# Optimization experiments

Hardware: AMD Instinct MI355X
Metric: run time of the kernel (lower is better)

The kernel has to match this reference:

```python
import jax, jax.numpy as jnp
import numpy as np

L = 12      # gpt2-small layers
D = 768     # n_embd
H = 12      # heads
NTOK = 60   # A5 group size / vocab
DST = 128   # d_state
B, T = 8, 1024
ID_ID = 0
INJECT = 8  # inject_layer


def _ln(x, g, b):
    m = x.mean(-1, keepdims=True)
    v = x.var(-1, keepdims=True)
    return (x - m) * jax.lax.rsqrt(v + 1e-5) * g + b


def _forward(tok_emb, state_emb, sp_w, sp_b, wh_w, wh_b, ws_w, ws_b, wd_w, wd_b,
             head_w, head_b, wpe, ln1_g, ln1_b, attn_w, attn_b, proj_w, proj_b,
             ln2_g, ln2_b, fc_w, fc_b, mproj_w, mproj_b, lnf_g, lnf_b,
             input_ids, mul):
    Bc, Tc = input_ids.shape
    # --- sequential group-recurrence state scan: s_{t+1} = mul[x_t, s_t] ---
    def step(s, ids_t):
        s2 = mul[ids_t, s]
        return s2, s2
    s0 = jnp.full((Bc,), ID_ID, jnp.int32)
    _, post = jax.lax.scan(step, s0, input_ids.T)   # [T, B] post-states
    post = post.T                                    # [B, T]
    pre = jnp.concatenate([jnp.full((Bc, 1), ID_ID, jnp.int32), post[:, :-1]], axis=1)
    # clean mode: inject PRE-states everywhere (mask == 1)
    s = state_emb[pre] @ sp_w + sp_b                 # [B, T, D] projected state channel
    # input_add injection
    x = tok_emb[input_ids] + s
    # --- frozen GPT-2 forward ---
    h = x + wpe[:Tc]
    hd = D // H
    scale = 1.0 / np.sqrt(hd)
    causal = jnp.tril(jnp.ones((Tc, Tc), bool))
    for l in range(L):
        a = _ln(h, ln1_g[l], ln1_b[l])
        qkv = a @ attn_w[l] + attn_b[l]
        q, k, v = jnp.split(qkv, 3, axis=-1)
        q = q.reshape(Bc, Tc, H, hd)
        k = k.reshape(Bc, Tc, H, hd)
        v = v.reshape(Bc, Tc, H, hd)
        sc = jnp.einsum('bthd,bshd->bhts', q, k) * scale
        sc = jnp.where(causal, sc, jnp.float32(-1e9))
        att = jax.nn.softmax(sc, axis=-1)
        o = jnp.einsum('bhts,bshd->bthd', att, v).reshape(Bc, Tc, D)
        h = h + o @ proj_w[l] + proj_b[l]
        m = _ln(h, ln2_g[l], ln2_b[l])
        h = h + jax.nn.gelu(m @ fc_w[l] + fc_b[l], approximate=True) @ mproj_w[l] + mproj_b[l]
        if l == INJECT:
            # gated residual fusion hook on block output
            gate = jax.nn.sigmoid(h @ wh_w + wh_b + s @ ws_w + ws_b)
            h = h + gate * (s @ wd_w + wd_b)
    h = _ln(h, lnf_g, lnf_b)
    logits = h[:, -1] @ head_w + head_b             # [B, NTOK]
    return logits


def setup_inputs() -> dict:
    key = jax.random.key(0)
    ks = iter(jax.random.split(key, 48))
    p = lambda *sh: (0.02 * jax.random.normal(next(ks), sh)).astype(jnp.float32)
    return dict(
        input_ids=jax.random.randint(next(ks), (B, T), 0, NTOK, jnp.int32),
        mul=jax.random.randint(next(ks), (NTOK, NTOK), 0, NTOK, jnp.int32),
        tok_emb=p(NTOK, D), state_emb=p(NTOK, DST),
        sp_w=p(DST, D), sp_b=jnp.zeros((D,), jnp.float32),
        wh_w=p(D, D), wh_b=jnp.zeros((D,), jnp.float32),
        ws_w=p(D, D), ws_b=jnp.zeros((D,), jnp.float32),
        wd_w=p(D, D), wd_b=jnp.zeros((D,), jnp.float32),
        head_w=p(D, NTOK), head_b=jnp.zeros((NTOK,), jnp.float32),
        wpe=p(T, D),
        ln1_g=jnp.ones((L, D), jnp.float32), ln1_b=jnp.zeros((L, D), jnp.float32),
        attn_w=p(L, D, 3 * D), attn_b=jnp.zeros((L, 3 * D), jnp.float32),
        proj_w=p(L, D, D), proj_b=jnp.zeros((L, D), jnp.float32),
        ln2_g=jnp.ones((L, D), jnp.float32), ln2_b=jnp.zeros((L, D), jnp.float32),
        fc_w=p(L, D, 4 * D), fc_b=jnp.zeros((L, 4 * D), jnp.float32),
        mproj_w=p(L, 4 * D, D), mproj_b=jnp.zeros((L, D), jnp.float32),
        lnf_g=jnp.ones((D,), jnp.float32), lnf_b=jnp.zeros((D,), jnp.float32),
    )


def reference(input_ids, mul, tok_emb, state_emb, sp_w, sp_b, wh_w, wh_b, ws_w, ws_b,
              wd_w, wd_b, head_w, head_b, wpe, ln1_g, ln1_b, attn_w, attn_b,
              proj_w, proj_b, ln2_g, ln2_b, fc_w, fc_b, mproj_w, mproj_b, lnf_g, lnf_b):
    return _forward(tok_emb, state_emb, sp_w, sp_b, wh_w, wh_b, ws_w, ws_b, wd_w, wd_b,
                    head_w, head_b, wpe, ln1_g, ln1_b, attn_w, attn_b, proj_w, proj_b,
                    ln2_g, ln2_b, fc_w, fc_b, mproj_w, mproj_b, lnf_g, lnf_b,
                    input_ids, mul)
```

## Files before the change

### kernel.cpp

```cpp
#include <hip/hip_runtime.h>
#include <hip/hip_bf16.h>
#include <math.h>

#define L_LAYERS 12
#define D_MODEL 768
#define H_HEADS 12
#define HD 64
#define NTOK 60
#define DST 128
#define BATCH 8
#define SEQ 1024
#define NT (BATCH * SEQ)
#define INJECT_L 8

typedef short bf16x8 __attribute__((ext_vector_type(8)));
typedef float f32x4 __attribute__((ext_vector_type(4)));
typedef unsigned short u16x4 __attribute__((ext_vector_type(4)));

__device__ __forceinline__ unsigned short f2bf(float f) {
    unsigned int u = __float_as_uint(f);
    u = (u + 0x7FFF + ((u >> 16) & 1)) >> 16;
    return (unsigned short)u;
}

__device__ __forceinline__ float gelu_fast(float x) {
    float two_c = 1.5957691216057308f * (x + 0.044715f * x * x * x);
    return x / (1.0f + __expf(-two_c));
}

__device__ __forceinline__ void async_copy16(void* lds, const void* gmem) {
    __builtin_amdgcn_global_load_lds(
        (const __attribute__((address_space(1))) unsigned int*)gmem,
        (__attribute__((address_space(3))) unsigned int*)lds,
        16, 0, 0);
}

__global__ __launch_bounds__(1024) void scan_kernel(const int* __restrict__ ids,
                                                    const int* __restrict__ mul,
                                                    int* __restrict__ pre) {
    __shared__ int smul[NTOK * NTOK];
    __shared__ int sids[SEQ];
    __shared__ int Mc[64 * NTOK];
    __shared__ int entry[64];
    int b = blockIdx.x;
    int tid = threadIdx.x;
    for (int i = tid; i < NTOK * NTOK; i += 1024) smul[i] = mul[i];
    for (int i = tid; i < SEQ; i += 1024) sids[i] = ids[b * SEQ + i];
    __syncthreads();
    for (int task = tid; task < 64 * NTOK; task += 1024) {
        int c = task / NTOK, s = task - c * NTOK;
        int st = s;
        #pragma unroll
        for (int j = 0; j < 16; j++) st = smul[sids[c * 16 + j] * NTOK + st];
        Mc[c * NTOK + s] = st;
    }
    __syncthreads();
    if (tid == 0) {
        int st = 0;
        for (int c = 0; c < 64; c++) { entry[c] = st; st = Mc[c * NTOK + st]; }
    }
    __syncthreads();
    if (tid < 64) {
        int c = tid;
        int st = entry[c];
        int* pr = pre + b * SEQ + c * 16;
        #pragma unroll
        for (int j = 0; j < 16; j++) {
            pr[j] = st;
            st = smul[sids[c * 16 + j] * NTOK + st];
        }
    }
}

__global__ __launch_bounds__(256) void state_table_kernel(const float* __restrict__ state_emb,
                                                          const float* __restrict__ sp_w,
                                                          const float* __restrict__ sp_b,
                                                          float* __restrict__ stable) {
    int st = blockIdx.x;
    __shared__ float se[DST];
    if (threadIdx.x < DST) se[threadIdx.x] = state_emb[st * DST + threadIdx.x];
    __syncthreads();
    for (int d = threadIdx.x; d < D_MODEL; d += 256) {
        float acc = sp_b[d];
        #pragma unroll 8
        for (int k = 0; k < DST; k++) acc += se[k] * sp_w[k * D_MODEL + d];
        stable[st * D_MODEL + d] = acc;
    }
}

__global__ __launch_bounds__(64) void embed_gather(const int* __restrict__ ids,
                                                   const int* __restrict__ pre,
                                                   const float* __restrict__ tok_emb,
                                                   const float* __restrict__ stable,
                                                   const float* __restrict__ wpe,
                                                   unsigned short* __restrict__ s_bf,
                                                   float* __restrict__ h) {
    int n = blockIdx.x;
    int t = n & (SEQ - 1);
    int lane = threadIdx.x;
    const float4* te = (const float4*)(tok_emb + (size_t)ids[n] * D_MODEL);
    const float4* sv = (const float4*)(stable + (size_t)pre[n] * D_MODEL);
    const float4* wp = (const float4*)(wpe + (size_t)t * D_MODEL);
    float4* hr = (float4*)(h + (size_t)n * D_MODEL);
    unsigned short* sr = s_bf + (size_t)n * D_MODEL;
    #pragma unroll
    for (int j = 0; j < 3; j++) {
        int idx = j * 64 + lane;
        float4 a = te[idx], b = sv[idx], c = wp[idx];
        float4 o;
        o.x = a.x + b.x + c.x; o.y = a.y + b.y + c.y;
        o.z = a.z + b.z + c.z; o.w = a.w + b.w + c.w;
        hr[idx] = o;
        u16x4 pk = { f2bf(b.x), f2bf(b.y), f2bf(b.z), f2bf(b.w) };
        *(u16x4*)&sr[idx * 4] = pk;
    }
}

__global__ __launch_bounds__(256) void ln_bf16_kernel(const float* __restrict__ x,
                                                      const float* __restrict__ g,
                                                      const float* __restrict__ bta,
                                                      unsigned short* __restrict__ out) {
    int row = blockIdx.x * 4 + (threadIdx.x >> 6);
    int lane = threadIdx.x & 63;
    const float4* xr = (const float4*)(x + (size_t)row * D_MODEL);
    float4 v[3];
    float sum = 0.f, sq = 0.f;
    #pragma unroll
    for (int j = 0; j < 3; j++) {
        v[j] = xr[j * 64 + lane];
        sum += v[j].x + v[j].y + v[j].z + v[j].w;
        sq += v[j].x * v[j].x + v[j].y * v[j].y + v[j].z * v[j].z + v[j].w * v[j].w;
    }
    for (int off = 32; off; off >>= 1) {
        sum += __shfl_xor(sum, off);
        sq += __shfl_xor(sq, off);
    }
    float mean = sum * (1.0f / D_MODEL);
    float var = sq * (1.0f / D_MODEL) - mean * mean;
    float r = rsqrtf(var + 1e-5f);
    const float4* g4 = (const float4*)g;
    const float4* b4 = (const float4*)bta;
    unsigned short* orow = out + (size_t)row * D_MODEL;
    #pragma unroll
    for (int j = 0; j < 3; j++) {
        int idx = j * 64 + lane;
        float4 gg = g4[idx], bb = b4[idx];
        u16x4 pk = { f2bf((v[j].x - mean) * r * gg.x + bb.x),
                     f2bf((v[j].y - mean) * r * gg.y + bb.y),
                     f2bf((v[j].z - mean) * r * gg.z + bb.z),
                     f2bf((v[j].w - mean) * r * gg.w + bb.w) };
        *(u16x4*)&orow[idx * 4] = pk;
    }
}

__global__ __launch_bounds__(256) void ln_f32_kernel(const float* __restrict__ x,
                                                     const float* __restrict__ g,
                                                     const float* __restrict__ bta,
                                                     float* __restrict__ out,
                                                     long in_stride, long out_stride) {
    long row = blockIdx.x;
    const float* xr = x + row * in_stride;
    int tid = threadIdx.x;
    float v0 = xr[tid], v1 = xr[tid + 256], v2 = xr[tid + 512];
    float sum = v0 + v1 + v2;
    float sq = v0 * v0 + v1 * v1 + v2 * v2;
    for (int off = 32; off; off >>= 1) {
        sum += __shfl_xor(sum, off);
        sq += __shfl_xor(sq, off);
    }
    __shared__ float red[8];
    int wid = tid >> 6;
    if ((tid & 63) == 0) { red[wid] = sum; red[4 + wid] = sq; }
    __syncthreads();
    sum = red[0] + red[1] + red[2] + red[3];
    sq = red[4] + red[5] + red[6] + red[7];
    float mean = sum * (1.0f / D_MODEL);
    float var = sq * (1.0f / D_MODEL) - mean * mean;
    float r = rsqrtf(var + 1e-5f);
    float* orow = out + row * out_stride;
    orow[tid] = (v0 - mean) * r * g[tid] + bta[tid];
    orow[tid + 256] = (v1 - mean) * r * g[tid + 256] + bta[tid + 256];
    orow[tid + 512] = (v2 - mean) * r * g[tid + 512] + bta[tid + 512];
}

__device__ __forceinline__ void conv_tile(const float* __restrict__ src,
                                          unsigned short* __restrict__ dst,
                                          int R, int C, int rt, int ct,
                                          int tc, int tr) {
    __shared__ float tile[32][33];
    int r0 = rt * 32, c0 = ct * 32;
    #pragma unroll
    for (int i = 0; i < 32; i += 8)
        tile[tr + i][tc] = src[(size_t)(r0 + tr + i) * C + c0 + tc];
    __syncthreads();
    #pragma unroll
    for (int i = 0; i < 32; i += 8)
        dst[(size_t)(c0 + tr + i) * R + r0 + tc] = f2bf(tile[tc][tr + i]);
}

__global__ __launch_bounds__(256) void wconv_layer(const float* __restrict__ attn_w,
                                                   const float* __restrict__ proj_w,
                                                   const float* __restrict__ fc_w,
                                                   const float* __restrict__ mproj_w,
                                                   unsigned short* __restrict__ attn_wt,
                                                   unsigned short* __restrict__ proj_wt,
                                                   unsigned short* __restrict__ fc_wt,
                                                   unsigned short* __restrict__ mproj_wt) {
    int bid = blockIdx.x;
    const float* src; unsigned short* dst; int R, C, CT, tloc;
    if (bid < 1728)      { src = attn_w;  dst = attn_wt;  R = 768;  C = 2304; CT = 72; tloc = bid; }
    else if (bid < 2304) { src = proj_w;  dst = proj_wt;  R = 768;  C = 768;  CT = 24; tloc = bid - 1728; }
    else if (bid < 4608) { src = fc_w;    dst = fc_wt;    R = 768;  C = 3072; CT = 96; tloc = bid - 2304; }
    else                 { src = mproj_w; dst = mproj_wt; R = 3072; C = 768;  CT = 24; tloc = bid - 4608; }
    int rt = tloc / CT, ct = tloc - rt * CT;
    conv_tile(src, dst, R, C, rt, ct, threadIdx.x, threadIdx.y);
}

__global__ __launch_bounds__(256) void wconv_inject(const float* __restrict__ wh_w,
                                                    const float* __restrict__ ws_w,
                                                    const float* __restrict__ wd_w,
                                                    unsigned short* __restrict__ wh_t,
                                                    unsigned short* __restrict__ ws_t,
                                                    unsigned short* __restrict__ wd_t) {
    int bid = blockIdx.x;
    int sel = bid / 576, tloc = bid - sel * 576;
    const float* src = sel == 0 ? wh_w : (sel == 1 ? ws_w : wd_w);
    unsigned short* dst = sel == 0 ? wh_t : (sel == 1 ? ws_t : wd_t);
    int rt = tloc / 24, ct = tloc - rt * 24;
    conv_tile(src, dst, 768, 768, rt, ct, threadIdx.x, threadIdx.y);
}

#define FLAG_OUTBF16 1
#define FLAG_GELU 2
#define FLAG_RESID 4
#define FLAG_MIRROR 8

__global__ __launch_bounds__(256) void mfma_gemm(const unsigned short* __restrict__ A,
                                                 const unsigned short* __restrict__ Wt,
                                                 const float* __restrict__ bias,
                                                 const float* __restrict__ residual,
                                                 float* __restrict__ Cf,
                                                 unsigned short* __restrict__ Cb,
                                                 unsigned short* __restrict__ Cmir,
                                                 int M, int K, int N, int flags) {
    __shared__ unsigned short As[128 * 64];
    __shared__ unsigned short Bs[128 * 64];
    int tid = threadIdx.x;
    int wave = tid >> 6, lane = tid & 63;
    int quad = lane >> 4, l16 = lane & 15;
    int m0 = blockIdx.x * 128, n0 = blockIdx.y * 128;
    int wm = (wave & 1) * 64, wn = (wave >> 1) * 64;
    f32x4 acc[4][4] = {};

    for (int k0 = 0; k0 < K; k0 += 64) {
        #pragma unroll
        for (int i = 0; i < 4; i++) {
            int chunk = i * 256 + wave * 64 + lane;
            int r = chunk >> 3;
            int cc = (chunk & 7) ^ (r & 7);
            async_copy16(&As[(i * 256 + wave * 64) * 8],
                         A + (size_t)(m0 + r) * K + k0 + cc * 8);
            async_copy16(&Bs[(i * 256 + wave * 64) * 8],
                         Wt + (size_t)(n0 + r) * K + k0 + cc * 8);
        }
        __syncthreads();
        #pragma unroll
        for (int sub = 0; sub < 2; sub++) {
            bf16x8 af[4], bfr[4];
            #pragma unroll
            for (int mi = 0; mi < 4; mi++) {
                int R = wm + mi * 16 + l16;
                int slot = (sub * 4 + quad) ^ (R & 7);
                af[mi] = *(const bf16x8*)&As[R * 64 + slot * 8];
            }
            #pragma unroll
            for (int ni = 0; ni < 4; ni++) {
                int R = wn + ni * 16 + l16;
                int slot = (sub * 4 + quad) ^ (R & 7);
                bfr[ni] = *(const bf16x8*)&Bs[R * 64 + slot * 8];
            }
            #pragma unroll
            for (int mi = 0; mi < 4; mi++)
                #pragma unroll
                for (int ni = 0; ni < 4; ni++)
                    acc[mi][ni] = __builtin_amdgcn_mfma_f32_16x16x32_bf16(
                        af[mi], bfr[ni], acc[mi][ni], 0, 0, 0);
        }
        __syncthreads();
    }
    #pragma unroll
    for (int mi = 0; mi < 4; mi++) {
        #pragma unroll
        for (int ni = 0; ni < 4; ni++) {
            int col = n0 + wn + ni * 16 + l16;
            float bv = bias[col];
            #pragma unroll
            for (int r = 0; r < 4; r++) {
                int row = m0 + wm + mi * 16 + quad * 4 + r;
                size_t idx = (size_t)row * N + col;
                float v = acc[mi][ni][r] + bv;
                if (flags & FLAG_RESID) v += residual[idx];
                if (flags & FLAG_GELU) v = gelu_fast(v);
                if (flags & FLAG_OUTBF16) Cb[idx] = f2bf(v);
                else Cf[idx] = v;
                if (flags & FLAG_MIRROR) Cmir[idx] = f2bf(v);
            }
        }
    }
}

__global__ __launch_bounds__(256) void attn_mfma(const unsigned short* __restrict__ qkv,
                                                 unsigned short* __restrict__ o) {
    int qt = gridDim.x - 1 - blockIdx.x;
    int hh = blockIdx.y, b = blockIdx.z;
    int tid = threadIdx.x, wave = tid >> 6, lane = tid & 63;
    int quad = lane >> 4, l16 = lane & 15;
    __shared__ unsigned short Qs[64][72];
    __shared__ unsigned short Ks[64][72];
    __shared__ unsigned short Vt[64][72];
    __shared__ unsigned short Ps[4][16][72];
    const size_t rstride = 3 * D_MODEL;
    int q0 = qt * 64;

    {
        size_t qbase = ((size_t)(b * SEQ + q0)) * rstride + hh * HD;
        #pragma unroll
        for (int i = 0; i < 2; i++) {
            int chunk = i * 256 + tid;
            int r = chunk >> 3, cc = chunk & 7;
            *(uint4*)&Qs[r][cc * 8] =
                *(const uint4*)(qkv + qbase + (size_t)r * rstride + cc * 8);
        }
    }

    float m_r[4] = {-1e30f, -1e30f, -1e30f, -1e30f};
    float l_r[4] = {0.f, 0.f, 0.f, 0.f};
    f32x4 oacc[4] = {};

    for (int kt = 0; kt <= qt; kt++) {
        int kb = kt * 64;
        __syncthreads();
        size_t kbase = ((size_t)(b * SEQ + kb)) * rstride + D_MODEL + hh * HD;
        size_t vbase = ((size_t)(b * SEQ + kb)) * rstride + 2 * D_MODEL + hh * HD;
        #pragma unroll
        for (int i = 0; i < 2; i++) {
            int chunk = i * 256 + tid;
            int r = chunk >> 3, cc = chunk & 7;
            *(uint4*)&Ks[r][cc * 8] =
                *(const uint4*)(qkv + kbase + (size_t)r * rstride + cc * 8);
        }
        #pragma unroll
        for (int i = 0; i < 2; i++) {
            int key = lane;
            int dg = i * 4 + wave;
            uint4 vv = *(const uint4*)(qkv + vbase + (size_t)key * rstride + dg * 8);
            const unsigned short* vs = (const unsigned short*)&vv;
            #pragma unroll
            for (int j = 0; j < 8; j++) Vt[dg * 8 + j][key] = vs[j];
        }
        __syncthreads();

        f32x4 sacc[4] = {};
        bf16x8 qf0 = *(const bf16x8*)&Qs[wave * 16 + l16][quad * 8];
        bf16x8 qf1 = *(const bf16x8*)&Qs[wave * 16 + l16][32 + quad * 8];
        #pragma unroll
        for (int ni = 0; ni < 4; ni++) {
            bf16x8 kf0 = *(const bf16x8*)&Ks[ni * 16 + l16][quad * 8];
            bf16x8 kf1 = *(const bf16x8*)&Ks[ni * 16 + l16][32 + quad * 8];
            sacc[ni] = __builtin_amdgcn_mfma_f32_16x16x32_bf16(qf0, kf0, sacc[ni], 0, 0, 0);
            sacc[ni] = __builtin_amdgcn_mfma_f32_16x16x32_bf16(qf1, kf1, sacc[ni], 0, 0, 0);
        }

        bool diag = (kt == qt);
        const float scale = 0.125f;
        #pragma unroll
        for (int r = 0; r < 4; r++) {
            int qrow_loc = wave * 16 + quad * 4 + r;
            float mx = m_r[r];
            #pragma unroll
            for (int ni = 0; ni < 4; ni++) {
                float sv = sacc[ni][r] * scale;
                if (diag && (ni * 16 + l16 > qrow_loc)) sv = -1e30f;
                sacc[ni][r] = sv;
                mx = fmaxf(mx, sv);
            }
            for (int off = 8; off; off >>= 1) mx = fmaxf(mx, __shfl_xor(mx, off));
            float alpha = __expf(m_r[r] - mx);
            m_r[r] = mx;
            float ls = 0.f;
            #pragma unroll
            for (int ni = 0; ni < 4; ni++) {
                float p = __expf(sacc[ni][r] - mx);
                sacc[ni][r] = p;
                ls += p;
            }
            for (int off = 8; off; off >>= 1) ls += __shfl_xor(ls, off);
            l_r[r] = l_r[r] * alpha + ls;
            #pragma unroll
            for (int ni = 0; ni < 4; ni++) oacc[ni][r] *= alpha;
        }

        #pragma unroll
        for (int ni = 0; ni < 4; ni++)
            #pragma unroll
            for (int r = 0; r < 4; r++)
                Ps[wave][quad * 4 + r][ni * 16 + l16] = f2bf(sacc[ni][r]);
        asm volatile("s_waitcnt lgkmcnt(0)" ::: "memory");

        bf16x8 pf0 = *(const bf16x8*)&Ps[wave][l16][quad * 8];
        bf16x8 pf1 = *(const bf16x8*)&Ps[wave][l16][32 + quad * 8];
        #pragma unroll
        for (int ni = 0; ni < 4; ni++) {
            bf16x8 vf0 = *(const bf16x8*)&Vt[ni * 16 + l16][quad * 8];
            bf16x8 vf1 = *(const bf16x8*)&Vt[ni * 16 + l16][32 + quad * 8];
            oacc[ni] = __builtin_amdgcn_mfma_f32_16x16x32_bf16(pf0, vf0, oacc[ni], 0, 0, 0);
            oacc[ni] = __builtin_amdgcn_mfma_f32_16x16x32_bf16(pf1, vf1, oacc[ni], 0, 0, 0);
        }
    }

    #pragma unroll
    for (int ni = 0; ni < 4; ni++) {
        #pragma unroll
        for (int r = 0; r < 4; r++) {
            float inv = 1.0f / l_r[r];
            int row = q0 + wave * 16 + quad * 4 + r;
            o[((size_t)(b * SEQ + row)) * D_MODEL + hh * HD + ni * 16 + l16] =
                f2bf(oacc[ni][r] * inv);
        }
    }
}

__global__ __launch_bounds__(256) void gate_kernel(float* __restrict__ h,
                                                   const float* __restrict__ z,
                                                   const float* __restrict__ dv,
                                                   size_t total) {
    size_t i = (size_t)blockIdx.x * blockDim.x + threadIdx.x;
    size_t stride = (size_t)gridDim.x * blockDim.x;
    for (; i < total; i += stride) {
        float g = 1.0f / (1.0f + __expf(-z[i]));
        h[i] += g * dv[i];
    }
}

__global__ __launch_bounds__(64) void head_kernel(const float* __restrict__ hn,
                                                  const float* __restrict__ head_w,
                                                  const float* __restrict__ head_b,
                                                  float* __restrict__ out) {
    int b = blockIdx.x;
    int n = threadIdx.x;
    if (n < NTOK) {
        float acc = head_b[n];
        const float* hr = hn + b * D_MODEL;
        for (int k = 0; k < D_MODEL; k++) acc += hr[k] * head_w[k * NTOK + n];
        out[b * NTOK + n] = acc;
    }
}

extern "C" void kernel_launch(void* const* d_in, const int* in_sizes, int n_in,
                              void* d_out, int out_size, void* d_ws, size_t ws_size,
                              hipStream_t stream) {
    (void)in_sizes; (void)n_in; (void)out_size; (void)ws_size;
    const int* input_ids = (const int*)d_in[0];
    const int* mul       = (const int*)d_in[1];
    const float* tok_emb = (const float*)d_in[2];
    const float* state_emb = (const float*)d_in[3];
    const float* sp_w = (const float*)d_in[4];
    const float* sp_b = (const float*)d_in[5];
    const float* wh_w = (const float*)d_in[6];
    const float* wh_b = (const float*)d_in[7];
    const float* ws_w = (const float*)d_in[8];
    const float* ws_b = (const float*)d_in[9];
    const float* wd_w = (const float*)d_in[10];
    const float* wd_b = (const float*)d_in[11];
    const float* head_w = (const float*)d_in[12];
    const float* head_b = (const float*)d_in[13];
    const float* wpe  = (const float*)d_in[14];
    const float* ln1_g = (const float*)d_in[15];
    const float* ln1_b = (const float*)d_in[16];
    const float* attn_w = (const float*)d_in[17];
    const float* attn_b = (const float*)d_in[18];
    const float* proj_w = (const float*)d_in[19];
    const float* proj_b = (const float*)d_in[20];
    const float* ln2_g = (const float*)d_in[21];
    const float* ln2_b = (const float*)d_in[22];
    const float* fc_w = (const float*)d_in[23];
    const float* fc_b = (const float*)d_in[24];
    const float* mproj_w = (const float*)d_in[25];
    const float* mproj_b = (const float*)d_in[26];
    const float* lnf_g = (const float*)d_in[27];
    const float* lnf_b = (const float*)d_in[28];
    float* out = (float*)d_out;

    size_t off = 0;
    auto alloc = [&](size_t bytes) {
        void* p = (char*)d_ws + off;
        off += (bytes + 255) & ~(size_t)255;
        return p;
    };
    int* pre = (int*)alloc((size_t)NT * 4);
    float* stable = (float*)alloc((size_t)NTOK * D_MODEL * 4);
    unsigned short* s_bf   = (unsigned short*)alloc((size_t)NT * D_MODEL * 2);
    float* h               = (float*)alloc((size_t)NT * D_MODEL * 4);
    unsigned short* a_bf   = (unsigned short*)alloc((size_t)NT * D_MODEL * 2);
    unsigned short* qkv_bf = (unsigned short*)alloc((size_t)NT * 3 * D_MODEL * 2);
    unsigned short* u_bf   = (unsigned short*)alloc((size_t)NT * 4 * D_MODEL * 2);
    unsigned short* h8_bf  = (unsigned short*)alloc((size_t)NT * D_MODEL * 2);
    float* z  = (float*)alloc((size_t)NT * D_MODEL * 4);
    float* dv = (float*)alloc((size_t)NT * D_MODEL * 4);
    float* hn = (float*)alloc((size_t)BATCH * D_MODEL * 4);
    unsigned short* attn_wt  = (unsigned short*)alloc((size_t)2304 * 768 * 2);
    unsigned short* proj_wt  = (unsigned short*)alloc((size_t)768 * 768 * 2);
    unsigned short* fc_wt    = (unsigned short*)alloc((size_t)3072 * 768 * 2);
    unsigned short* mproj_wt = (unsigned short*)alloc((size_t)768 * 3072 * 2);
    unsigned short* wh_t = (unsigned short*)alloc((size_t)768 * 768 * 2);
    unsigned short* ws_t = (unsigned short*)alloc((size_t)768 * 768 * 2);
    unsigned short* wd_t = (unsigned short*)alloc((size_t)768 * 768 * 2);

    scan_kernel<<<BATCH, 1024, 0, stream>>>(input_ids, mul, pre);
    state_table_kernel<<<NTOK, 256, 0, stream>>>(state_emb, sp_w, sp_b, stable);
    embed_gather<<<NT, 64, 0, stream>>>(input_ids, pre, tok_emb, stable, wpe, s_bf, h);
    wconv_inject<<<1728, dim3(32, 8), 0, stream>>>(wh_w, ws_w, wd_w, wh_t, ws_t, wd_t);

    for (int l = 0; l < L_LAYERS; l++) {
        wconv_layer<<<6912, dim3(32, 8), 0, stream>>>(
            attn_w + (size_t)l * 768 * 2304, proj_w + (size_t)l * 768 * 768,
            fc_w + (size_t)l * 768 * 3072, mproj_w + (size_t)l * 3072 * 768,
            attn_wt, proj_wt, fc_wt, mproj_wt);

        ln_bf16_kernel<<<NT / 4, 256, 0, stream>>>(h, ln1_g + l * D_MODEL,
                                                   ln1_b + l * D_MODEL, a_bf);
        mfma_gemm<<<dim3(NT / 128, 2304 / 128), 256, 0, stream>>>(
            a_bf, attn_wt, attn_b + (size_t)l * 2304, nullptr,
            nullptr, qkv_bf, nullptr, NT, 768, 2304, FLAG_OUTBF16);
        attn_mfma<<<dim3(SEQ / 64, H_HEADS, BATCH), 256, 0, stream>>>(qkv_bf, a_bf);
        mfma_gemm<<<dim3(NT / 128, 768 / 128), 256, 0, stream>>>(
            a_bf, proj_wt, proj_b + (size_t)l * 768, h,
            h, nullptr, nullptr, NT, 768, 768, FLAG_RESID);
        ln_bf16_kernel<<<NT / 4, 256, 0, stream>>>(h, ln2_g + l * D_MODEL,
                                                   ln2_b + l * D_MODEL, a_bf);
        mfma_gemm<<<dim3(NT / 128, 3072 / 128), 256, 0, stream>>>(
            a_bf, fc_wt, fc_b + (size_t)l * 3072, nullptr,
            nullptr, u_bf, nullptr, NT, 768, 3072, FLAG_OUTBF16 | FLAG_GELU);
        int mpflags = FLAG_RESID | (l == INJECT_L ? FLAG_MIRROR : 0);
        mfma_gemm<<<dim3(NT / 128, 768 / 128), 256, 0, stream>>>(
            u_bf, mproj_wt, mproj_b + (size_t)l * 768, h,
            h, nullptr, h8_bf, NT, 3072, 768, mpflags);

        if (l == INJECT_L) {
            mfma_gemm<<<dim3(NT / 128, 768 / 128), 256, 0, stream>>>(
                h8_bf, wh_t, wh_b, nullptr, z, nullptr, nullptr, NT, 768, 768, 0);
            mfma_gemm<<<dim3(NT / 128, 768 / 128), 256, 0, stream>>>(
                s_bf, ws_t, ws_b, z, z, nullptr, nullptr, NT, 768, 768, FLAG_RESID);
            mfma_gemm<<<dim3(NT / 128, 768 / 128), 256, 0, stream>>>(
                s_bf, wd_t, wd_b, nullptr, dv, nullptr, nullptr, NT, 768, 768, 0);
            gate_kernel<<<dim3(2048), 256, 0, stream>>>(h, z, dv, (size_t)NT * D_MODEL);
        }
    }

    ln_f32_kernel<<<BATCH, 256, 0, stream>>>(h + (size_t)(SEQ - 1) * D_MODEL,
                                             lnf_g, lnf_b, hn,
                                             (long)SEQ * D_MODEL, D_MODEL);
    head_kernel<<<BATCH, 64, 0, stream>>>(hn, head_w, head_b, out);
}
```

Baseline: 4.568 ms.

## Double attention query tile and keep Q fragments in registers

The attention kernel now processes 128 query rows per block, with each wave owning two 16-row blocks. Q fragments stay in registers instead of LDS, and each K/V tile load is shared across twice as many query rows. V fragments are loaded once per tile and reused for both row blocks. The V transpose uses a permuted column order so P can be stored as packed 4-element writes. MFMA sections are bracketed with s_setprio. The cost is half as many blocks and a coarser causal load imbalance, plus more register pressure.

```diff
diff --git a/kernel.cpp b/kernel.cpp
--- a/kernel.cpp
+++ b/kernel.cpp
@@ -315,29 +315,30 @@
     int hh = blockIdx.y, b = blockIdx.z;
     int tid = threadIdx.x, wave = tid >> 6, lane = tid & 63;
     int quad = lane >> 4, l16 = lane & 15;
-    __shared__ unsigned short Qs[64][72];
     __shared__ unsigned short Ks[64][72];
     __shared__ unsigned short Vt[64][72];
-    __shared__ unsigned short Ps[4][16][72];
+    __shared__ unsigned short Ps[4][2][16][72];
     const size_t rstride = 3 * D_MODEL;
-    int q0 = qt * 64;
-
-    {
-        size_t qbase = ((size_t)(b * SEQ + q0)) * rstride + hh * HD;
-        #pragma unroll
-        for (int i = 0; i < 2; i++) {
-            int chunk = i * 256 + tid;
-            int r = chunk >> 3, cc = chunk & 7;
-            *(uint4*)&Qs[r][cc * 8] =
-                *(const uint4*)(qkv + qbase + (size_t)r * rstride + cc * 8);
-        }
-    }
-
-    float m_r[4] = {-1e30f, -1e30f, -1e30f, -1e30f};
-    float l_r[4] = {0.f, 0.f, 0.f, 0.f};
-    f32x4 oacc[4] = {};
-
-    for (int kt = 0; kt <= qt; kt++) {
+    int q0 = qt * 128;
+    int rb0 = q0 + wave * 32;
+
+    bf16x8 qf[2][2];
+    #pragma unroll
+    for (int mb = 0; mb < 2; mb++) {
+        int row = rb0 + mb * 16 + l16;
+        const unsigned short* qp = qkv + ((size_t)(b * SEQ + row)) * rstride + hh * HD;
+        qf[mb][0] = *(const bf16x8*)(qp + quad * 8);
+        qf[mb][1] = *(const bf16x8*)(qp + 32 + quad * 8);
+    }
+
+    float m_r[2][4] = {{-1e30f, -1e30f, -1e30f, -1e30f},
+                       {-1e30f, -1e30f, -1e30f, -1e30f}};
+    float l_r[2][4] = {{0.f, 0.f, 0.f, 0.f}, {0.f, 0.f, 0.f, 0.f}};
+    f32x4 oacc[2][4] = {};
+
+    int vc = 4 * (lane & 15) + (lane >> 4);
+    int nkt = 2 * qt + 2;
+    for (int kt = 0; kt < nkt; kt++) {
         int kb = kt * 64;
         __syncthreads();
         size_t kbase = ((size_t)(b * SEQ + kb)) * rstride + D_MODEL + hh * HD;
@@ -351,81 +352,95 @@
         }
         #pragma unroll
         for (int i = 0; i < 2; i++) {
-            int key = lane;
             int dg = i * 4 + wave;
-            uint4 vv = *(const uint4*)(qkv + vbase + (size_t)key * rstride + dg * 8);
+            uint4 vv = *(const uint4*)(qkv + vbase + (size_t)lane * rstride + dg * 8);
             const unsigned short* vs = (const unsigned short*)&vv;
             #pragma unroll
-            for (int j = 0; j < 8; j++) Vt[dg * 8 + j][key] = vs[j];
+            for (int j = 0; j < 8; j++) Vt[dg * 8 + j][vc] = vs[j];
         }
         __syncthreads();
 
-        f32x4 sacc[4] = {};
-        bf16x8 qf0 = *(const bf16x8*)&Qs[wave * 16 + l16][quad * 8];
-        bf16x8 qf1 = *(const bf16x8*)&Qs[wave * 16 + l16][32 + quad * 8];
+        if (kb > rb0 + 31) continue;
+
+        bf16x8 vf[4][2];
         #pragma unroll
         for (int ni = 0; ni < 4; ni++) {
-            bf16x8 kf0 = *(const bf16x8*)&Ks[ni * 16 + l16][quad * 8];
-            bf16x8 kf1 = *(const bf16x8*)&Ks[ni * 16 + l16][32 + quad * 8];
-            sacc[ni] = __builtin_amdgcn_mfma_f32_16x16x32_bf16(qf0, kf0, sacc[ni], 0, 0, 0);
-            sacc[ni] = __builtin_amdgcn_mfma_f32_16x16x32_bf16(qf1, kf1, sacc[ni], 0, 0, 0);
-        }
-
-        bool diag = (kt == qt);
-        const float scale = 0.125f;
-        #pragma unroll
-        for (int r = 0; r < 4; r++) {
-            int qrow_loc = wave * 16 + quad * 4 + r;
-            float mx = m_r[r];
+            vf[ni][0] = *(const bf16x8*)&Vt[ni * 16 + l16][quad * 8];
+            vf[ni][1] = *(const bf16x8*)&Vt[ni * 16 + l16][32 + quad * 8];
+        }
+
+        #pragma unroll
+        for (int mb = 0; mb < 2; mb++) {
+            int rbase = rb0 + mb * 16;
+            if (kb > rbase + 15) continue;
+
+            f32x4 sacc[4] = {};
+            __builtin_amdgcn_s_setprio(1);
             #pragma unroll
             for (int ni = 0; ni < 4; ni++) {
-                float sv = sacc[ni][r] * scale;
-                if (diag && (ni * 16 + l16 > qrow_loc)) sv = -1e30f;
-                sacc[ni][r] = sv;
-                mx = fmaxf(mx, sv);
-            }
-            for (int off = 8; off; off >>= 1) mx = fmaxf(mx, __shfl_xor(mx, off));
-            float alpha = __expf(m_r[r] - mx);
-            m_r[r] = mx;
-            float ls = 0.f;
+                bf16x8 kf0 = *(const bf16x8*)&Ks[ni * 16 + l16][quad * 8];
+                bf16x8 kf1 = *(const bf16x8*)&Ks[ni * 16 + l16][32 + quad * 8];
+                sacc[ni] = __builtin_amdgcn_mfma_f32_16x16x32_bf16(qf[mb][0], kf0, sacc[ni], 0, 0, 0);
+                sacc[ni] = __builtin_amdgcn_mfma_f32_16x16x32_bf16(qf[mb][1], kf1, sacc[ni], 0, 0, 0);
+            }
+            __builtin_amdgcn_s_setprio(0);
+
+            bool tail = (kb + 63 > rbase);
+            const float scale = 0.125f;
+            #pragma unroll
+            for (int r = 0; r < 4; r++) {
+                int row_abs = rbase + quad * 4 + r;
+                float mx = m_r[mb][r];
+                #pragma unroll
+                for (int ni = 0; ni < 4; ni++) {
+                    float sv = sacc[ni][r] * scale;
+                    if (tail && (kb + ni * 16 + l16 > row_abs)) sv = -1e30f;
+                    sacc[ni][r] = sv;
+                    mx = fmaxf(mx, sv);
+                }
+                for (int off = 8; off; off >>= 1) mx = fmaxf(mx, __shfl_xor(mx, off));
+                float alpha = __expf(m_r[mb][r] - mx);
+                m_r[mb][r] = mx;
+                float ls = 0.f;
+                #pragma unroll
+                for (int ni = 0; ni < 4; ni++) {
+                    float p = __expf(sacc[ni][r] - mx);
+                    sacc[ni][r] = p;
+                    ls += p;
+                }
+                for (int off = 8; off; off >>= 1) ls += __shfl_xor(ls, off);
+                l_r[mb][r] = l_r[mb][r] * alpha + ls;
+                #pragma unroll
+                for (int ni = 0; ni < 4; ni++) oacc[mb][ni][r] *= alpha;
+                u16x4 pk = { f2bf(sacc[0][r]), f2bf(sacc[1][r]),
+                             f2bf(sacc[2][r]), f2bf(sacc[3][r]) };
+                *(u16x4*)&Ps[wave][mb][quad * 4 + r][l16 * 4] = pk;
+            }
+            asm volatile("s_waitcnt lgkmcnt(0)" ::: "memory");
+
+            bf16x8 pf0 = *(const bf16x8*)&Ps[wave][mb][l16][quad * 8];
+            bf16x8 pf1 = *(const bf16x8*)&Ps[wave][mb][l16][32 + quad * 8];
+            __builtin_amdgcn_s_setprio(1);
             #pragma unroll
             for (int ni = 0; ni < 4; ni++) {
-                float p = __expf(sacc[ni][r] - mx);
-                sacc[ni][r] = p;
-                ls += p;
-            }
-            for (int off = 8; off; off >>= 1) ls += __shfl_xor(ls, off);
-            l_r[r] = l_r[r] * alpha + ls;
-            #pragma unroll
-            for (int ni = 0; ni < 4; ni++) oacc[ni][r] *= alpha;
-        }
-
-        #pragma unroll
-        for (int ni = 0; ni < 4; ni++)
-            #pragma unroll
-            for (int r = 0; r < 4; r++)
-                Ps[wave][quad * 4 + r][ni * 16 + l16] = f2bf(sacc[ni][r]);
-        asm volatile("s_waitcnt lgkmcnt(0)" ::: "memory");
-
-        bf16x8 pf0 = *(const bf16x8*)&Ps[wave][l16][quad * 8];
-        bf16x8 pf1 = *(const bf16x8*)&Ps[wave][l16][32 + quad * 8];
+                oacc[mb][ni] = __builtin_amdgcn_mfma_f32_16x16x32_bf16(pf0, vf[ni][0], oacc[mb][ni], 0, 0, 0);
+                oacc[mb][ni] = __builtin_amdgcn_mfma_f32_16x16x32_bf16(pf1, vf[ni][1], oacc[mb][ni], 0, 0, 0);
+            }
+            __builtin_amdgcn_s_setprio(0);
+        }
+    }
+
+    #pragma unroll
+    for (int mb = 0; mb < 2; mb++) {
         #pragma unroll
         for (int ni = 0; ni < 4; ni++) {
-            bf16x8 vf0 = *(const bf16x8*)&Vt[ni * 16 + l16][quad * 8];
-            bf16x8 vf1 = *(const bf16x8*)&Vt[ni * 16 + l16][32 + quad * 8];
-            oacc[ni] = __builtin_amdgcn_mfma_f32_16x16x32_bf16(pf0, vf0, oacc[ni], 0, 0, 0);
-            oacc[ni] = __builtin_amdgcn_mfma_f32_16x16x32_bf16(pf1, vf1, oacc[ni], 0, 0, 0);
-        }
-    }
-
-    #pragma unroll
-    for (int ni = 0; ni < 4; ni++) {
-        #pragma unroll
-        for (int r = 0; r < 4; r++) {
-            float inv = 1.0f / l_r[r];
-            int row = q0 + wave * 16 + quad * 4 + r;
-            o[((size_t)(b * SEQ + row)) * D_MODEL + hh * HD + ni * 16 + l16] =
-                f2bf(oacc[ni][r] * inv);
+            #pragma unroll
+            for (int r = 0; r < 4; r++) {
+                float inv = 1.0f / l_r[mb][r];
+                int row = rb0 + mb * 16 + quad * 4 + r;
+                o[((size_t)(b * SEQ + row)) * D_MODEL + hh * HD + ni * 16 + l16] =
+                    f2bf(oacc[mb][ni][r] * inv);
+            }
         }
     }
 }
@@ -532,7 +547,7 @@
         mfma_gemm<<<dim3(NT / 128, 2304 / 128), 256, 0, stream>>>(
             a_bf, attn_wt, attn_b + (size_t)l * 2304, nullptr,
             nullptr, qkv_bf, nullptr, NT, 768, 2304, FLAG_OUTBF16);
-        attn_mfma<<<dim3(SEQ / 64, H_HEADS, BATCH), 256, 0, stream>>>(qkv_bf, a_bf);
+        attn_mfma<<<dim3(SEQ / 128, H_HEADS, BATCH), 256, 0, stream>>>(qkv_bf, a_bf);
         mfma_gemm<<<dim3(NT / 128, 768 / 128), 256, 0, stream>>>(
             a_bf, proj_wt, proj_b + (size_t)l * 768, h,
             h, nullptr, nullptr, NT, 768, 768, FLAG_RESID);
```

Measured after the change: 5.007 ms. +9.6%, slower.

## Prefetch K/V tiles into registers and transpose QK MFMA layout in attention

Applied to the files above, without the earlier changes.

The attention kernel now register-prefetches the next K/V tile while the current one is computed, hiding global load latency behind MFMA work. Q fragments are loaded straight into registers, which removes the Q shared-memory tile. The QK^T MFMA operands are swapped so each lane holds scores for one query row, letting row max and sum reductions happen mostly in registers with two cross-lane shuffles. P is written to LDS as packed 4-element vectors, and s_setprio raises wave priority around MFMA blocks. The cost is extra registers for prefetch buffers and the alpha/l redistribution shuffles.

```diff
diff --git a/kernel.cpp b/kernel.cpp
--- a/kernel.cpp
+++ b/kernel.cpp
@@ -315,100 +315,136 @@
     int hh = blockIdx.y, b = blockIdx.z;
     int tid = threadIdx.x, wave = tid >> 6, lane = tid & 63;
     int quad = lane >> 4, l16 = lane & 15;
-    __shared__ unsigned short Qs[64][72];
     __shared__ unsigned short Ks[64][72];
     __shared__ unsigned short Vt[64][72];
     __shared__ unsigned short Ps[4][16][72];
     const size_t rstride = 3 * D_MODEL;
     int q0 = qt * 64;
 
+    int qrow = q0 + wave * 16 + l16;
+    const unsigned short* qp = qkv + ((size_t)(b * SEQ + qrow)) * rstride + hh * HD;
+    bf16x8 qf0 = *(const bf16x8*)(qp + quad * 8);
+    bf16x8 qf1 = *(const bf16x8*)(qp + 32 + quad * 8);
+
+    float m_r = -1e30f, l_r = 0.f;
+    f32x4 oacc[4] = {};
+
+    uint4 kreg[2], vreg[2];
     {
-        size_t qbase = ((size_t)(b * SEQ + q0)) * rstride + hh * HD;
+        size_t kbase = ((size_t)(b * SEQ)) * rstride + D_MODEL + hh * HD;
+        size_t vbase = kbase + D_MODEL;
         #pragma unroll
         for (int i = 0; i < 2; i++) {
             int chunk = i * 256 + tid;
             int r = chunk >> 3, cc = chunk & 7;
-            *(uint4*)&Qs[r][cc * 8] =
-                *(const uint4*)(qkv + qbase + (size_t)r * rstride + cc * 8);
-        }
-    }
-
-    float m_r[4] = {-1e30f, -1e30f, -1e30f, -1e30f};
-    float l_r[4] = {0.f, 0.f, 0.f, 0.f};
-    f32x4 oacc[4] = {};
+            kreg[i] = *(const uint4*)(qkv + kbase + (size_t)r * rstride + cc * 8);
+        }
+        #pragma unroll
+        for (int i = 0; i < 2; i++) {
+            int dg = i * 4 + wave;
+            vreg[i] = *(const uint4*)(qkv + vbase + (size_t)lane * rstride + dg * 8);
+        }
+    }
 
     for (int kt = 0; kt <= qt; kt++) {
-        int kb = kt * 64;
         __syncthreads();
-        size_t kbase = ((size_t)(b * SEQ + kb)) * rstride + D_MODEL + hh * HD;
-        size_t vbase = ((size_t)(b * SEQ + kb)) * rstride + 2 * D_MODEL + hh * HD;
         #pragma unroll
         for (int i = 0; i < 2; i++) {
             int chunk = i * 256 + tid;
             int r = chunk >> 3, cc = chunk & 7;
-            *(uint4*)&Ks[r][cc * 8] =
-                *(const uint4*)(qkv + kbase + (size_t)r * rstride + cc * 8);
+            *(uint4*)&Ks[r][cc * 8] = kreg[i];
         }
         #pragma unroll
         for (int i = 0; i < 2; i++) {
-            int key = lane;
             int dg = i * 4 + wave;
-            uint4 vv = *(const uint4*)(qkv + vbase + (size_t)key * rstride + dg * 8);
+            uint4 vv = vreg[i];
             const unsigned short* vs = (const unsigned short*)&vv;
             #pragma unroll
-            for (int j = 0; j < 8; j++) Vt[dg * 8 + j][key] = vs[j];
+            for (int j = 0; j < 8; j++) Vt[dg * 8 + j][lane] = vs[j];
+        }
+        if (kt < qt) {
+            size_t kbase = ((size_t)(b * SEQ + (kt + 1) * 64)) * rstride + D_MODEL + hh * HD;
+            size_t vbase = kbase + D_MODEL;
+            #pragma unroll
+            for (int i = 0; i < 2; i++) {
+                int chunk = i * 256 + tid;
+                int r = chunk >> 3, cc = chunk & 7;
+                kreg[i] = *(const uint4*)(qkv + kbase + (size_t)r * rstride + cc * 8);
+            }
+            #pragma unroll
+            for (int i = 0; i < 2; i++) {
+                int dg = i * 4 + wave;
+                vreg[i] = *(const uint4*)(qkv + vbase + (size_t)lane * rstride + dg * 8);
+            }
         }
         __syncthreads();
 
         f32x4 sacc[4] = {};
-        bf16x8 qf0 = *(const bf16x8*)&Qs[wave * 16 + l16][quad * 8];
-        bf16x8 qf1 = *(const bf16x8*)&Qs[wave * 16 + l16][32 + quad * 8];
+        __builtin_amdgcn_s_setprio(1);
         #pragma unroll
         for (int ni = 0; ni < 4; ni++) {
             bf16x8 kf0 = *(const bf16x8*)&Ks[ni * 16 + l16][quad * 8];
             bf16x8 kf1 = *(const bf16x8*)&Ks[ni * 16 + l16][32 + quad * 8];
-            sacc[ni] = __builtin_amdgcn_mfma_f32_16x16x32_bf16(qf0, kf0, sacc[ni], 0, 0, 0);
-            sacc[ni] = __builtin_amdgcn_mfma_f32_16x16x32_bf16(qf1, kf1, sacc[ni], 0, 0, 0);
-        }
+            sacc[ni] = __builtin_amdgcn_mfma_f32_16x16x32_bf16(kf0, qf0, sacc[ni], 0, 0, 0);
+            sacc[ni] = __builtin_amdgcn_mfma_f32_16x16x32_bf16(kf1, qf1, sacc[ni], 0, 0, 0);
+        }
+        __builtin_amdgcn_s_setprio(0);
 
         bool diag = (kt == qt);
         const float scale = 0.125f;
-        #pragma unroll
-        for (int r = 0; r < 4; r++) {
-            int qrow_loc = wave * 16 + quad * 4 + r;
-            float mx = m_r[r];
-            #pragma unroll
-            for (int ni = 0; ni < 4; ni++) {
-                float sv = sacc[ni][r] * scale;
-                if (diag && (ni * 16 + l16 > qrow_loc)) sv = -1e30f;
-                sacc[ni][r] = sv;
-                mx = fmaxf(mx, sv);
+        int qloc = wave * 16 + l16;
+        float mxg[4];
+        #pragma unroll
+        for (int ni = 0; ni < 4; ni++) {
+            #pragma unroll
+            for (int r = 0; r < 4; r++) {
+                float s = sacc[ni][r] * scale;
+                if (diag && (ni * 16 + quad * 4 + r > qloc)) s = -1e30f;
+                sacc[ni][r] = s;
             }
-            for (int off = 8; off; off >>= 1) mx = fmaxf(mx, __shfl_xor(mx, off));
-            float alpha = __expf(m_r[r] - mx);
-            m_r[r] = mx;
-            float ls = 0.f;
-            #pragma unroll
-            for (int ni = 0; ni < 4; ni++) {
+            mxg[ni] = fmaxf(fmaxf(sacc[ni][0], sacc[ni][1]),
+                            fmaxf(sacc[ni][2], sacc[ni][3]));
+        }
+        float mx = fmaxf(fmaxf(mxg[0], mxg[1]), fmaxf(mxg[2], mxg[3]));
+        mx = fmaxf(mx, m_r);
+        mx = fmaxf(mx, __shfl_xor(mx, 16));
+        mx = fmaxf(mx, __shfl_xor(mx, 32));
+        float alpha = __expf(m_r - mx);
+        m_r = mx;
+        float lsg[4];
+        #pragma unroll
+        for (int ni = 0; ni < 4; ni++) {
+            #pragma unroll
+            for (int r = 0; r < 4; r++) {
                 float p = __expf(sacc[ni][r] - mx);
                 sacc[ni][r] = p;
-                ls += p;
             }
-            for (int off = 8; off; off >>= 1) ls += __shfl_xor(ls, off);
-            l_r[r] = l_r[r] * alpha + ls;
-            #pragma unroll
-            for (int ni = 0; ni < 4; ni++) oacc[ni][r] *= alpha;
-        }
-
+            lsg[ni] = (sacc[ni][0] + sacc[ni][1]) + (sacc[ni][2] + sacc[ni][3]);
+        }
+        float ls = (lsg[0] + lsg[1]) + (lsg[2] + lsg[3]);
+        ls += __shfl_xor(ls, 16);
+        ls += __shfl_xor(ls, 32);
+        l_r = l_r * alpha + ls;
+
+        float at[4];
+        #pragma unroll
+        for (int r = 0; r < 4; r++) at[r] = __shfl(alpha, quad * 4 + r);
         #pragma unroll
         for (int ni = 0; ni < 4; ni++)
             #pragma unroll
-            for (int r = 0; r < 4; r++)
-                Ps[wave][quad * 4 + r][ni * 16 + l16] = f2bf(sacc[ni][r]);
+            for (int r = 0; r < 4; r++) oacc[ni][r] *= at[r];
+
+        #pragma unroll
+        for (int ni = 0; ni < 4; ni++) {
+            u16x4 pk = { f2bf(sacc[ni][0]), f2bf(sacc[ni][1]),
+                         f2bf(sacc[ni][2]), f2bf(sacc[ni][3]) };
+            *(u16x4*)&Ps[wave][l16][ni * 16 + quad * 4] = pk;
+        }
         asm volatile("s_waitcnt lgkmcnt(0)" ::: "memory");
 
         bf16x8 pf0 = *(const bf16x8*)&Ps[wave][l16][quad * 8];
         bf16x8 pf1 = *(const bf16x8*)&Ps[wave][l16][32 + quad * 8];
+        __builtin_amdgcn_s_setprio(1);
         #pragma unroll
         for (int ni = 0; ni < 4; ni++) {
             bf16x8 vf0 = *(const bf16x8*)&Vt[ni * 16 + l16][quad * 8];
@@ -416,16 +452,19 @@
             oacc[ni] = __builtin_amdgcn_mfma_f32_16x16x32_bf16(pf0, vf0, oacc[ni], 0, 0, 0);
             oacc[ni] = __builtin_amdgcn_mfma_f32_16x16x32_bf16(pf1, vf1, oacc[ni], 0, 0, 0);
         }
-    }
-
+        __builtin_amdgcn_s_setprio(0);
+    }
+
+    float lt[4];
+    #pragma unroll
+    for (int r = 0; r < 4; r++) lt[r] = 1.0f / __shfl(l_r, quad * 4 + r);
     #pragma unroll
     for (int ni = 0; ni < 4; ni++) {
         #pragma unroll
         for (int r = 0; r < 4; r++) {
-            float inv = 1.0f / l_r[r];
             int row = q0 + wave * 16 + quad * 4 + r;
             o[((size_t)(b * SEQ + row)) * D_MODEL + hh * HD + ni * 16 + l16] =
-                f2bf(oacc[ni][r] * inv);
+                f2bf(oacc[ni][r] * lt[r]);
         }
     }
 }
```

After: 4.447 ms. 1.03x faster.
